# Kernel optimization log

Measured on AMD Instinct MI355X. Metric: run time of the kernel, lower is better.

The kernel has to match this reference:

```python
import jax, jax.numpy as jnp
import numpy as np

N = 2_000_000   # number of inversion targets
H = 64          # hidden width, arch = [1, H, H, 1]
MONO = 1e-3     # monotonic_const
N_ITER = 20     # bisection depth


def _apply_layers(x, pre_w1, b1, pre_w2, b2, pre_w3, b3):
    # PositiveLinear(A_constraint='exp') + Sigmoid stack; final layer also exp+sigmoid.
    h = jax.nn.sigmoid(x @ jnp.exp(pre_w1).T + b1)   # [N, H]
    h = jax.nn.sigmoid(h @ jnp.exp(pre_w2).T + b2)   # [N, H]
    y = jax.nn.sigmoid(h @ jnp.exp(pre_w3).T + b3)   # [N, 1]
    # d == 1, non_conditional_dim == 0 -> x[:, 0:1] == x
    return y + MONO * x


def setup_inputs() -> dict:
    key = jax.random.key(0)
    ks = jax.random.split(key, 7)

    def u(k, shape, lo, hi):
        return jax.random.uniform(k, shape, dtype=jnp.float32) * (hi - lo) + lo

    # exp-constraint init: pre_weight ~ U[log(0.01), log(sqrt(1/in_features))]
    lo1, hi1 = np.log(0.01), np.log(np.sqrt(1.0 / 1.0))
    loH, hiH = np.log(0.01), np.log(np.sqrt(1.0 / H))
    pre_w1 = u(ks[0], (H, 1), lo1, hi1)
    b1 = u(ks[1], (H,), -1.0, 1.0)            # scale = 1/in_features = 1
    pre_w2 = u(ks[2], (H, H), loH, hiH)
    b2 = u(ks[3], (H,), -1.0 / H, 1.0 / H)
    pre_w3 = u(ks[4], (1, H), loH, hiH)
    b3 = u(ks[5], (1,), -1.0 / H, 1.0 / H)
    z = jax.random.uniform(ks[6], (N, 1), dtype=jnp.float32)  # CDF targets in (0,1)
    return dict(z=z, pre_w1=pre_w1, b1=b1, pre_w2=pre_w2, b2=b2,
                pre_w3=pre_w3, b3=b3)


def reference(z, pre_w1, b1, pre_w2, b2, pre_w3, b3):
    A = lambda x: _apply_layers(x, pre_w1, b1, pre_w2, b2, pre_w3, b3)
    # scale(): F(x) = (A(x) - A(start)) / (A(end) - A(start)); d==1 so start=0, end=1
    a0 = A(jnp.zeros((1, 1), jnp.float32))
    a1 = A(jnp.ones((1, 1), jnp.float32))
    F = lambda q: (A(q) - a0) / (a1 - a0)

    # bisection_search: 20 interval halvings, return final midpoint (elementwise,
    # vectorized over the per-sample loop in the original F_inv)
    def body(_, carry):
        lo, hi = carry
        mid = (lo + hi) * 0.5
        gt = F(mid) > z
        return (jnp.where(gt, lo, mid), jnp.where(gt, mid, hi))

    lo, hi = jax.lax.fori_loop(0, N_ITER, body,
                               (jnp.zeros_like(z), jnp.ones_like(z)))
    return (lo + hi) * 0.5
```

## Files before the change

kernel.cpp:

```cpp
#include <hip/hip_runtime.h>


#define MONO 1e-3f
#define TLOG2 13
#define TSZ (1 << TLOG2)
#define KLOG2 16
#define KSZ (1 << KLOG2)

#define WS_WE2 0
#define WS_WE1 4096
#define WS_WE3 (4096 + 64)
#define WS_T   (4096 + 128)
#define WS_G   (WS_T + TSZ + 1)

typedef float fvec64 __attribute__((ext_vector_type(64)));

__device__ __forceinline__ float fast_rcp(float x) {
#if __has_builtin(__builtin_amdgcn_rcpf)
    return __builtin_amdgcn_rcpf(x);
#else
    return 1.0f / x;
#endif
}

__device__ __forceinline__ float sigmoidf_(float t) {
    return fast_rcp(1.0f + __expf(-t));
}

__global__ __launch_bounds__(256) void exp_weights_kernel(
        const float* __restrict__ pw1,
        const float* __restrict__ pw2,
        const float* __restrict__ pw3,
        float* __restrict__ ws) {
    int i = blockIdx.x * blockDim.x + threadIdx.x;
    if (i < 4096) ws[WS_WE2 + i] = expf(pw2[i]);
    if (i < 64) {
        ws[WS_WE1 + i] = expf(pw1[i]);
        ws[WS_WE3 + i] = expf(pw3[i]);
    }
}

__global__ __launch_bounds__(256, 4) void build_table_kernel(
        const float* __restrict__ b1,
        const float* __restrict__ b2,
        const float* __restrict__ b3,
        const float* __restrict__ ws,
        float* __restrict__ T) {
    const float* __restrict__ WE2 = ws + WS_WE2;
    const float* __restrict__ WE1 = ws + WS_WE1;
    const float* __restrict__ WE3 = ws + WS_WE3;

    int tid  = threadIdx.x;
    int lane = tid & 63;
    int sub = __builtin_amdgcn_readfirstlane(tid >> 6);
    int j = blockIdx.x * 64 + lane;
    int jc = j <= TSZ ? j : TSZ;
    float x = (float)jc * (1.0f / (float)TSZ);

    fvec64 h1;
#pragma unroll
    for (int k = 0; k < 64; ++k)
        h1[k] = sigmoidf_(fmaf(x, WE1[k], b1[k]));

    const float* __restrict__ w2base = WE2 + sub * (16 * 64);
    const float* __restrict__ b2base = b2 + sub * 16;
    const float* __restrict__ w3base = WE3 + sub * 16;
    float acc3 = 0.0f;
#pragma unroll
    for (int r = 0; r < 16; ++r) {
        float acc = b2base[r];
        const float* __restrict__ wrow = w2base + r * 64;
#pragma unroll
        for (int jj = 0; jj < 64; ++jj)
            acc = fmaf(wrow[jj], h1[jj], acc);
        acc3 = fmaf(w3base[r], sigmoidf_(acc), acc3);
    }

    __shared__ float part[256];
    part[sub * 64 + lane] = acc3;
    __syncthreads();
    if (tid < 64 && j <= TSZ) {
        float s = part[lane] + part[64 + lane] + part[128 + lane]
                + part[192 + lane] + b3[0];
        T[j] = sigmoidf_(s) + MONO * x;
    }
}

__global__ __launch_bounds__(256) void invert_table_kernel(
        const float* __restrict__ T,
        float* __restrict__ G) {
    int k = blockIdx.x * blockDim.x + threadIdx.x;
    if (k > KSZ) return;
    float a0 = T[0];
    float a1 = T[TSZ];
    float zt = fmaf((float)k * (1.0f / (float)KSZ), a1 - a0, a0);

    int lo = 0;
#pragma unroll
    for (int s = TSZ >> 1; s >= 1; s >>= 1) {
        int cand = lo + s;
        if (T[cand] <= zt) lo = cand;
    }
    float tl = T[lo];
    float th = T[lo + 1];
    float d = th - tl;
    float t = (d > 1e-30f) ? (zt - tl) / d : 0.5f;
    t = fminf(fmaxf(t, 0.0f), 1.0f);
    G[k] = ((float)lo + t) * (1.0f / (float)TSZ);
}

__device__ __forceinline__ float apply_one(float zv, const float* __restrict__ G) {
    float u = zv * (float)KSZ;
    u = fminf(fmaxf(u, 0.0f), (float)KSZ);
    int k = (int)u;
    if (k > KSZ - 1) k = KSZ - 1;
    float frac = u - (float)k;
    float g0 = G[k];
    float g1 = G[k + 1];
    return fmaf(frac, g1 - g0, g0);
}

__global__ __launch_bounds__(256) void apply_kernel(
        const float* __restrict__ z,
        const float* __restrict__ G,
        float* __restrict__ out, int n) {
    int i = blockIdx.x * blockDim.x + threadIdx.x;
    int base = i * 4;
    if (base + 3 < n) {
        float4 zz = *reinterpret_cast<const float4*>(z + base);
        float4 oo;
        oo.x = apply_one(zz.x, G);
        oo.y = apply_one(zz.y, G);
        oo.z = apply_one(zz.z, G);
        oo.w = apply_one(zz.w, G);
        *reinterpret_cast<float4*>(out + base) = oo;
    } else {
        for (int t = base; t < n; ++t)
            out[t] = apply_one(z[t], G);
    }
}

extern "C" void kernel_launch(void* const* d_in, const int* in_sizes, int n_in,
                              void* d_out, int out_size, void* d_ws, size_t ws_size,
                              hipStream_t stream) {
    const float* z   = (const float*)d_in[0];
    const float* pw1 = (const float*)d_in[1];
    const float* b1  = (const float*)d_in[2];
    const float* pw2 = (const float*)d_in[3];
    const float* b2  = (const float*)d_in[4];
    const float* pw3 = (const float*)d_in[5];
    const float* b3  = (const float*)d_in[6];
    float* out = (float*)d_out;
    float* ws  = (float*)d_ws;
    int n = in_sizes[0];

    exp_weights_kernel<<<16, 256, 0, stream>>>(pw1, pw2, pw3, ws);
    build_table_kernel<<<(TSZ + 1 + 63) / 64, 256, 0, stream>>>(
        b1, b2, b3, ws, ws + WS_T);
    invert_table_kernel<<<(KSZ + 1 + 255) / 256, 256, 0, stream>>>(
        ws + WS_T, ws + WS_G);
    int nv = (n + 3) / 4;
    apply_kernel<<<(nv + 255) / 256, 256, 0, stream>>>(z, ws + WS_G, out, n);
}
```

Measured before the change: 106.6 us.

## Fuse weight exp into table build and search forward table directly in LDS

Folds the weight-exponentiation kernel into the table build kernel: each block exponentiates W2 into shared memory and computes W1/W3 exponentials inline. The inverse-table kernel and the interpolation kernel are replaced by one persistent apply kernel. It copies the forward table into LDS and runs a 13-step binary search per sample with linear interpolation. This cuts two launches and the inverse-table pass. In exchange each sample now does a 13-step dependent LDS search instead of two global gathers, and every build block recomputes 4096 exponentials.

```diff
diff --git a/kernel.cpp b/kernel.cpp
--- a/kernel.cpp
+++ b/kernel.cpp
@@ -4,14 +4,6 @@
 #define MONO 1e-3f
 #define TLOG2 13
 #define TSZ (1 << TLOG2)
-#define KLOG2 16
-#define KSZ (1 << KLOG2)
-
-#define WS_WE2 0
-#define WS_WE1 4096
-#define WS_WE3 (4096 + 64)
-#define WS_T   (4096 + 128)
-#define WS_G   (WS_T + TSZ + 1)
 
 typedef float fvec64 __attribute__((ext_vector_type(64)));
 
@@ -27,30 +19,25 @@
     return fast_rcp(1.0f + __expf(-t));
 }
 
-__global__ __launch_bounds__(256) void exp_weights_kernel(
+__global__ __launch_bounds__(256, 4) void fused_build_kernel(
         const float* __restrict__ pw1,
+        const float* __restrict__ b1,
         const float* __restrict__ pw2,
+        const float* __restrict__ b2,
         const float* __restrict__ pw3,
-        float* __restrict__ ws) {
-    int i = blockIdx.x * blockDim.x + threadIdx.x;
-    if (i < 4096) ws[WS_WE2 + i] = expf(pw2[i]);
-    if (i < 64) {
-        ws[WS_WE1 + i] = expf(pw1[i]);
-        ws[WS_WE3 + i] = expf(pw3[i]);
-    }
-}
-
-__global__ __launch_bounds__(256, 4) void build_table_kernel(
-        const float* __restrict__ b1,
-        const float* __restrict__ b2,
         const float* __restrict__ b3,
-        const float* __restrict__ ws,
         float* __restrict__ T) {
-    const float* __restrict__ WE2 = ws + WS_WE2;
-    const float* __restrict__ WE1 = ws + WS_WE1;
-    const float* __restrict__ WE3 = ws + WS_WE3;
+    __shared__ __align__(16) float W2s[4096];
+    __shared__ float part[256];
 
     int tid  = threadIdx.x;
+#pragma unroll
+    for (int i = 0; i < 16; ++i) {
+        int idx = tid + i * 256;
+        W2s[idx] = __expf(pw2[idx]);
+    }
+    __syncthreads();
+
     int lane = tid & 63;
     int sub = __builtin_amdgcn_readfirstlane(tid >> 6);
     int j = blockIdx.x * 64 + lane;
@@ -60,23 +47,26 @@
     fvec64 h1;
 #pragma unroll
     for (int k = 0; k < 64; ++k)
-        h1[k] = sigmoidf_(fmaf(x, WE1[k], b1[k]));
+        h1[k] = sigmoidf_(fmaf(x, __expf(pw1[k]), b1[k]));
 
-    const float* __restrict__ w2base = WE2 + sub * (16 * 64);
-    const float* __restrict__ b2base = b2 + sub * 16;
-    const float* __restrict__ w3base = WE3 + sub * 16;
     float acc3 = 0.0f;
 #pragma unroll
     for (int r = 0; r < 16; ++r) {
-        float acc = b2base[r];
-        const float* __restrict__ wrow = w2base + r * 64;
+        int row = sub * 16 + r;
+        float acc = b2[row];
+        const float4* __restrict__ w4 =
+            reinterpret_cast<const float4*>(&W2s[row * 64]);
 #pragma unroll
-        for (int jj = 0; jj < 64; ++jj)
-            acc = fmaf(wrow[jj], h1[jj], acc);
-        acc3 = fmaf(w3base[r], sigmoidf_(acc), acc3);
+        for (int q = 0; q < 16; ++q) {
+            float4 w = w4[q];
+            acc = fmaf(w.x, h1[4 * q + 0], acc);
+            acc = fmaf(w.y, h1[4 * q + 1], acc);
+            acc = fmaf(w.z, h1[4 * q + 2], acc);
+            acc = fmaf(w.w, h1[4 * q + 3], acc);
+        }
+        acc3 = fmaf(__expf(pw3[row]), sigmoidf_(acc), acc3);
     }
 
-    __shared__ float part[256];
     part[sub * 64 + lane] = acc3;
     __syncthreads();
     if (tid < 64 && j <= TSZ) {
@@ -86,58 +76,57 @@
     }
 }
 
-__global__ __launch_bounds__(256) void invert_table_kernel(
-        const float* __restrict__ T,
-        float* __restrict__ G) {
-    int k = blockIdx.x * blockDim.x + threadIdx.x;
-    if (k > KSZ) return;
-    float a0 = T[0];
-    float a1 = T[TSZ];
-    float zt = fmaf((float)k * (1.0f / (float)KSZ), a1 - a0, a0);
-
+__device__ __forceinline__ float search_one(float zv, const float* Ts,
+                                            float a0, float scale) {
+    float zt = fmaf(zv, scale, a0);
     int lo = 0;
 #pragma unroll
     for (int s = TSZ >> 1; s >= 1; s >>= 1) {
-        int cand = lo + s;
-        if (T[cand] <= zt) lo = cand;
+        int c = lo + s;
+        lo = (Ts[c] <= zt) ? c : lo;
     }
-    float tl = T[lo];
-    float th = T[lo + 1];
+    float tl = Ts[lo];
+    float th = Ts[lo + 1];
     float d = th - tl;
-    float t = (d > 1e-30f) ? (zt - tl) / d : 0.5f;
+    float t = (d > 1e-30f) ? (zt - tl) * fast_rcp(d) : 0.5f;
     t = fminf(fmaxf(t, 0.0f), 1.0f);
-    G[k] = ((float)lo + t) * (1.0f / (float)TSZ);
+    return ((float)lo + t) * (1.0f / (float)TSZ);
 }
 
-__device__ __forceinline__ float apply_one(float zv, const float* __restrict__ G) {
-    float u = zv * (float)KSZ;
-    u = fminf(fmaxf(u, 0.0f), (float)KSZ);
-    int k = (int)u;
-    if (k > KSZ - 1) k = KSZ - 1;
-    float frac = u - (float)k;
-    float g0 = G[k];
-    float g1 = G[k + 1];
-    return fmaf(frac, g1 - g0, g0);
-}
+#define APPLY_BLOCKS 512
 
-__global__ __launch_bounds__(256) void apply_kernel(
+__global__ __launch_bounds__(256) void fused_apply_kernel(
         const float* __restrict__ z,
-        const float* __restrict__ G,
+        const float* __restrict__ T,
         float* __restrict__ out, int n) {
-    int i = blockIdx.x * blockDim.x + threadIdx.x;
-    int base = i * 4;
-    if (base + 3 < n) {
-        float4 zz = *reinterpret_cast<const float4*>(z + base);
+    __shared__ __align__(16) float Ts[TSZ + 1];
+    int tid = threadIdx.x;
+#pragma unroll
+    for (int i = 0; i < (TSZ / 4) / 256; ++i) {
+        int idx = tid + i * 256;
+        reinterpret_cast<float4*>(Ts)[idx] =
+            reinterpret_cast<const float4*>(T)[idx];
+    }
+    if (tid == 0) Ts[TSZ] = T[TSZ];
+    __syncthreads();
+
+    float a0 = Ts[0];
+    float scale = Ts[TSZ] - a0;
+
+    int nv = n >> 2;
+    int stride = gridDim.x * 256;
+    for (int idx = blockIdx.x * 256 + tid; idx < nv; idx += stride) {
+        float4 zz = reinterpret_cast<const float4*>(z)[idx];
         float4 oo;
-        oo.x = apply_one(zz.x, G);
-        oo.y = apply_one(zz.y, G);
-        oo.z = apply_one(zz.z, G);
-        oo.w = apply_one(zz.w, G);
-        *reinterpret_cast<float4*>(out + base) = oo;
-    } else {
-        for (int t = base; t < n; ++t)
-            out[t] = apply_one(z[t], G);
+        oo.x = search_one(zz.x, Ts, a0, scale);
+        oo.y = search_one(zz.y, Ts, a0, scale);
+        oo.z = search_one(zz.z, Ts, a0, scale);
+        oo.w = search_one(zz.w, Ts, a0, scale);
+        reinterpret_cast<float4*>(out)[idx] = oo;
     }
+    int base = nv * 4;
+    for (int t = base + blockIdx.x * 256 + tid; t < n; t += stride)
+        out[t] = search_one(z[t], Ts, a0, scale);
 }
 
 extern "C" void kernel_launch(void* const* d_in, const int* in_sizes, int n_in,
@@ -151,14 +140,10 @@
     const float* pw3 = (const float*)d_in[5];
     const float* b3  = (const float*)d_in[6];
     float* out = (float*)d_out;
-    float* ws  = (float*)d_ws;
+    float* T   = (float*)d_ws;
     int n = in_sizes[0];
 
-    exp_weights_kernel<<<16, 256, 0, stream>>>(pw1, pw2, pw3, ws);
-    build_table_kernel<<<(TSZ + 1 + 63) / 64, 256, 0, stream>>>(
-        b1, b2, b3, ws, ws + WS_T);
-    invert_table_kernel<<<(KSZ + 1 + 255) / 256, 256, 0, stream>>>(
-        ws + WS_T, ws + WS_G);
-    int nv = (n + 3) / 4;
-    apply_kernel<<<(nv + 255) / 256, 256, 0, stream>>>(z, ws + WS_G, out, n);
+    fused_build_kernel<<<(TSZ + 1 + 63) / 64, 256, 0, stream>>>(
+        pw1, b1, pw2, b2, pw3, b3, T);
+    fused_apply_kernel<<<APPLY_BLOCKS, 256, 0, stream>>>(z, T, out, n);
 }
```

Measured after the change: 99.87 us. -6.3%, faster.
